# Kernel optimization log

Measured on AMD Instinct MI355X. Metric: run time of the kernel, lower is better.

## Reference

```python
import jax, jax.numpy as jnp
import numpy as np

MARGIN = 0.3
NEG_FILL = -100.0
EPS = 1e-6


def setup_inputs() -> dict:
    key = jax.random.key(0)
    k1, k2, k3 = jax.random.split(key, 3)
    B, N, D = 256, 131072, 128
    xembs = jax.random.normal(k1, (B, D), dtype=jnp.float32)
    yembs = jax.random.normal(k2, (N, D), dtype=jnp.float32)
    pos_inds = jax.random.randint(k3, (B, 1), 0, N, dtype=jnp.int64)
    # target: multi-hot label matrix; positives marked 1 at pos_inds
    target = jnp.zeros((B, N), dtype=jnp.float32)
    target = target.at[jnp.arange(B)[:, None], pos_inds].set(1.0)
    return {"xembs": xembs, "yembs": yembs, "target": target,
            "pos_inds": pos_inds, "num_neg": 5}


def reference(xembs, yembs, target, pos_inds, num_neg):
    # sim: [B, N]
    sim = xembs @ yembs.T
    # positive similarities: [B, 1]
    sim_p = jnp.take_along_axis(sim, pos_inds, axis=1)
    # mask out positives, mine hardest negatives
    neg_sim = jnp.where(target < EPS, sim, NEG_FILL)
    _, idx = jax.lax.top_k(neg_sim, num_neg)          # [B, num_neg]
    sim_n = jnp.take_along_axis(sim, idx, axis=1)      # [B, num_neg]
    # hinge triplet loss
    loss = jnp.maximum(jnp.zeros_like(sim_n), sim_n - sim_p + MARGIN)
    mask = (loss != 0).astype(loss.dtype)
    prob = jax.nn.softmax(sim_n * mask, axis=1)
    return (loss * prob).mean()
```

## Files before the change

kernel.cpp:

```cpp
#include <hip/hip_runtime.h>

#define BROWS 256
#define NCOLS 131072
#define DDIM  128
#define K     5
#define MARGIN 0.3f

#define NBLK   512
#define CPB    (NCOLS / NBLK)
#define NIT    (CPB / 16)
#define TSTR   260

typedef __attribute__((ext_vector_type(8))) __bf16 bf16x8;
typedef __attribute__((ext_vector_type(8))) unsigned short us8;
typedef __attribute__((ext_vector_type(4))) float f32x4;

__device__ __forceinline__ unsigned short f2b(float f) {
    union { float f; unsigned u; } x; x.f = f;
    unsigned r = x.u + 0x7FFFu + ((x.u >> 16) & 1u);
    return (unsigned short)(r >> 16);
}

__device__ __forceinline__ bf16x8 cvt8(const float4& lo, const float4& hi) {
    us8 t;
    t[0] = f2b(lo.x); t[1] = f2b(lo.y); t[2] = f2b(lo.z); t[3] = f2b(lo.w);
    t[4] = f2b(hi.x); t[5] = f2b(hi.y); t[6] = f2b(hi.z); t[7] = f2b(hi.w);
    return __builtin_bit_cast(bf16x8, t);
}

__global__ __launch_bounds__(256, 2) void gemm_topk_kernel(
    const float* __restrict__ x, const float* __restrict__ y,
    const int* __restrict__ pos,
    float* __restrict__ cand_v, float* __restrict__ simp)
{
    __shared__ float simT[16 * TSTR];

    const int tid   = threadIdx.x;
    const int lane  = tid & 63;
    const int quad  = lane >> 4;
    const int l15   = lane & 15;
    const int wrow0 = tid & 192;
    const int col0  = blockIdx.x * CPB;

    bf16x8 af[4][4];
#pragma unroll
    for (int mt = 0; mt < 4; ++mt) {
        const float* xp = x + (size_t)(wrow0 + mt * 16 + l15) * DDIM + quad * 8;
#pragma unroll
        for (int s = 0; s < 4; ++s) {
            const float4 a0 = *(const float4*)(xp + s * 32);
            const float4 a1 = *(const float4*)(xp + s * 32 + 4);
            af[mt][s] = cvt8(a0, a1);
        }
    }

    const int myPos = pos[tid];
    float t5[K];
#pragma unroll
    for (int p = 0; p < K; ++p) t5[p] = -3.0e38f;

    const float* yb = y + (size_t)(col0 + l15) * DDIM + quad * 8;

    float4 cur[8], nxt[8];
#pragma unroll
    for (int s = 0; s < 4; ++s) {
        cur[2 * s]     = *(const float4*)(yb + s * 32);
        cur[2 * s + 1] = *(const float4*)(yb + s * 32 + 4);
    }

    for (int it = 0; it < NIT; ++it) {
        if (it + 1 < NIT) {
            const float* yn = yb + (size_t)(it + 1) * 16 * DDIM;
#pragma unroll
            for (int s = 0; s < 4; ++s) {
                nxt[2 * s]     = *(const float4*)(yn + s * 32);
                nxt[2 * s + 1] = *(const float4*)(yn + s * 32 + 4);
            }
        }

        bf16x8 bfrag[4];
#pragma unroll
        for (int s = 0; s < 4; ++s) bfrag[s] = cvt8(cur[2 * s], cur[2 * s + 1]);

        f32x4 acc[4];
#pragma unroll
        for (int mt = 0; mt < 4; ++mt) acc[mt] = (f32x4){0.f, 0.f, 0.f, 0.f};
#pragma unroll
        for (int s = 0; s < 4; ++s)
#pragma unroll
            for (int mt = 0; mt < 4; ++mt)
                acc[mt] = __builtin_amdgcn_mfma_f32_16x16x32_bf16(af[mt][s], bfrag[s], acc[mt], 0, 0, 0);

        {
            float* wp = &simT[l15 * TSTR + wrow0 + quad * 4];
#pragma unroll
            for (int mt = 0; mt < 4; ++mt)
                *(f32x4*)(wp + mt * 16) = acc[mt];
        }

        const int colbase = col0 + it * 16;
#pragma unroll
        for (int c = 0; c < 16; ++c) {
            const float v = simT[c * TSTR + tid];
            const int col = colbase + c;
            if (col == myPos) {
                simp[tid] = v;
            } else if (v > t5[K - 1]) {
                float nv = v;
#pragma unroll
                for (int p = 0; p < K; ++p) {
                    const bool gt = nv > t5[p];
                    const float tv = t5[p];
                    if (gt) { t5[p] = nv; nv = tv; }
                }
            }
        }

#pragma unroll
        for (int i = 0; i < 8; ++i) cur[i] = nxt[i];
    }

    float* cv = cand_v + ((size_t)blockIdx.x * BROWS + tid) * K;
#pragma unroll
    for (int p = 0; p < K; ++p) cv[p] = t5[p];
}

__device__ __forceinline__ void merge5(float* __restrict__ t5, const float* __restrict__ src) {
#pragma unroll
    for (int p = 0; p < K; ++p) {
        const float v = src[p];
        if (v > t5[K - 1]) {
            float nv = v;
#pragma unroll
            for (int u = 0; u < K; ++u) {
                const bool gt = nv > t5[u];
                const float tv = t5[u];
                if (gt) { t5[u] = nv; nv = tv; }
            }
        }
    }
}

__global__ __launch_bounds__(256) void reduce_kernel(
    const float* __restrict__ cand_v, const float* __restrict__ simp,
    float* __restrict__ row_loss)
{
    const int row = blockIdx.x;
    const int tid = threadIdx.x;
    __shared__ float sv[256 * K];

    float t5[K];
#pragma unroll
    for (int p = 0; p < K; ++p) t5[p] = -3.0e38f;

    merge5(t5, cand_v + ((size_t)tid * BROWS + row) * K);
    merge5(t5, cand_v + ((size_t)(tid + 256) * BROWS + row) * K);

#pragma unroll
    for (int p = 0; p < K; ++p) sv[tid * K + p] = t5[p];
    __syncthreads();

    for (int s = 128; s >= 1; s >>= 1) {
        if (tid < s) {
            merge5(t5, &sv[(tid + s) * K]);
#pragma unroll
            for (int p = 0; p < K; ++p) sv[tid * K + p] = t5[p];
        }
        __syncthreads();
    }

    if (tid == 0) {
        const float sp = simp[row];
        float loss[K], logit[K];
#pragma unroll
        for (int p = 0; p < K; ++p) {
            loss[p]  = fmaxf(0.f, t5[p] - sp + MARGIN);
            logit[p] = (loss[p] != 0.f) ? t5[p] : 0.f;
        }
        float mx = logit[0];
#pragma unroll
        for (int p = 1; p < K; ++p) mx = fmaxf(mx, logit[p]);
        float den = 0.f, num = 0.f;
#pragma unroll
        for (int p = 0; p < K; ++p) {
            const float e = __expf(logit[p] - mx);
            den += e;
            num += loss[p] * e;
        }
        row_loss[row] = num / den;
    }
}

__global__ __launch_bounds__(256) void final_kernel(const float* __restrict__ row_loss,
                                                    float* __restrict__ out)
{
    const int tid = threadIdx.x;
    __shared__ float red[256];
    red[tid] = row_loss[tid];
    __syncthreads();
    for (int s = 128; s >= 1; s >>= 1) {
        if (tid < s) red[tid] += red[tid + s];
        __syncthreads();
    }
    if (tid == 0) out[0] = red[0] * (1.0f / (BROWS * K));
}

extern "C" void kernel_launch(void* const* d_in, const int* in_sizes, int n_in,
                              void* d_out, int out_size, void* d_ws, size_t ws_size,
                              hipStream_t stream) {
    const float* x  = (const float*)d_in[0];
    const float* y  = (const float*)d_in[1];
    const int* pos  = (const int*)d_in[3];

    float* cand_v   = (float*)d_ws;
    float* simp     = cand_v + (size_t)NBLK * BROWS * K;
    float* row_loss = simp + BROWS;

    gemm_topk_kernel<<<dim3(NBLK), 256, 0, stream>>>(x, y, pos, cand_v, simp);
    reduce_kernel<<<dim3(BROWS), 256, 0, stream>>>(cand_v, simp, row_loss);
    final_kernel<<<dim3(1), 256, 0, stream>>>(row_loss, (float*)d_out);
}
```

Before: 246.0 us.

## Pre-convert embeddings to bf16, deepen prefetch, restructure top-k scan and fuse final reduction

A separate kernel converts y and x to bf16 once, so the GEMM kernel streams half the bytes and does no per-tile conversion. The fp32 prefetch pair becomes a 4-deep register ring, and the tile is stored row-major in shared memory so each thread scans its row with float4 loads and a max pre-check. The candidate layout is transposed to give coalesced reads in the reduce, and the final kernel is replaced by an atomicAdd after a memset. The cost is an extra pass that reads and writes all of y, plus a nondeterministic atomic summation order.

Result: slower. 256.0 us (+4.1%).

```diff
diff --git a/kernel.cpp b/kernel.cpp
--- a/kernel.cpp
+++ b/kernel.cpp
@@ -9,7 +9,8 @@
 #define NBLK   512
 #define CPB    (NCOLS / NBLK)
 #define NIT    (CPB / 16)
-#define TSTR   260
+#define RSTR   20
+#define DEPTH  4
 
 typedef __attribute__((ext_vector_type(8))) __bf16 bf16x8;
 typedef __attribute__((ext_vector_type(8))) unsigned short us8;
@@ -21,19 +22,35 @@
     return (unsigned short)(r >> 16);
 }
 
-__device__ __forceinline__ bf16x8 cvt8(const float4& lo, const float4& hi) {
+__global__ __launch_bounds__(256) void convert_kernel(
+    const float* __restrict__ y, const float* __restrict__ x,
+    unsigned short* __restrict__ yb, unsigned short* __restrict__ xb)
+{
+    const int gid = blockIdx.x * 256 + threadIdx.x;
+    const int NY = NCOLS * DDIM / 8;
+    const float* src;
+    unsigned short* dst;
+    int idx;
+    if (gid < NY) { src = y; dst = yb; idx = gid; }
+    else {
+        idx = gid - NY;
+        if (idx >= BROWS * DDIM / 8) return;
+        src = x; dst = xb;
+    }
+    const float4 a = *(const float4*)(src + (size_t)idx * 8);
+    const float4 b = *(const float4*)(src + (size_t)idx * 8 + 4);
     us8 t;
-    t[0] = f2b(lo.x); t[1] = f2b(lo.y); t[2] = f2b(lo.z); t[3] = f2b(lo.w);
-    t[4] = f2b(hi.x); t[5] = f2b(hi.y); t[6] = f2b(hi.z); t[7] = f2b(hi.w);
-    return __builtin_bit_cast(bf16x8, t);
+    t[0] = f2b(a.x); t[1] = f2b(a.y); t[2] = f2b(a.z); t[3] = f2b(a.w);
+    t[4] = f2b(b.x); t[5] = f2b(b.y); t[6] = f2b(b.z); t[7] = f2b(b.w);
+    *(us8*)(dst + (size_t)idx * 8) = t;
 }
 
 __global__ __launch_bounds__(256, 2) void gemm_topk_kernel(
-    const float* __restrict__ x, const float* __restrict__ y,
+    const unsigned short* __restrict__ xb, const unsigned short* __restrict__ yb,
     const int* __restrict__ pos,
     float* __restrict__ cand_v, float* __restrict__ simp)
 {
-    __shared__ float simT[16 * TSTR];
+    __shared__ float simT[BROWS * RSTR];
 
     const int tid   = threadIdx.x;
     const int lane  = tid & 63;
@@ -45,13 +62,10 @@
     bf16x8 af[4][4];
 #pragma unroll
     for (int mt = 0; mt < 4; ++mt) {
-        const float* xp = x + (size_t)(wrow0 + mt * 16 + l15) * DDIM + quad * 8;
-#pragma unroll
-        for (int s = 0; s < 4; ++s) {
-            const float4 a0 = *(const float4*)(xp + s * 32);
-            const float4 a1 = *(const float4*)(xp + s * 32 + 4);
-            af[mt][s] = cvt8(a0, a1);
-        }
+        const unsigned short* xp = xb + (size_t)(wrow0 + mt * 16 + l15) * DDIM + quad * 8;
+#pragma unroll
+        for (int s = 0; s < 4; ++s)
+            af[mt][s] = __builtin_bit_cast(bf16x8, *(const us8*)(xp + s * 32));
     }
 
     const int myPos = pos[tid];
@@ -59,68 +73,74 @@
 #pragma unroll
     for (int p = 0; p < K; ++p) t5[p] = -3.0e38f;
 
-    const float* yb = y + (size_t)(col0 + l15) * DDIM + quad * 8;
-
-    float4 cur[8], nxt[8];
-#pragma unroll
-    for (int s = 0; s < 4; ++s) {
-        cur[2 * s]     = *(const float4*)(yb + s * 32);
-        cur[2 * s + 1] = *(const float4*)(yb + s * 32 + 4);
-    }
-
-    for (int it = 0; it < NIT; ++it) {
-        if (it + 1 < NIT) {
-            const float* yn = yb + (size_t)(it + 1) * 16 * DDIM;
+    const unsigned short* ybase = yb + (size_t)(col0 + l15) * DDIM + quad * 8;
+
+    us8 buf[DEPTH][4];
+#pragma unroll
+    for (int d = 0; d < DEPTH; ++d)
+#pragma unroll
+        for (int s = 0; s < 4; ++s)
+            buf[d][s] = *(const us8*)(ybase + (size_t)d * 16 * DDIM + s * 32);
+
+    for (int it0 = 0; it0 < NIT; it0 += DEPTH) {
+#pragma unroll
+        for (int d = 0; d < DEPTH; ++d) {
+            const int it = it0 + d;
+
+            f32x4 acc[4];
+#pragma unroll
+            for (int mt = 0; mt < 4; ++mt) acc[mt] = (f32x4){0.f, 0.f, 0.f, 0.f};
 #pragma unroll
             for (int s = 0; s < 4; ++s) {
-                nxt[2 * s]     = *(const float4*)(yn + s * 32);
-                nxt[2 * s + 1] = *(const float4*)(yn + s * 32 + 4);
-            }
-        }
-
-        bf16x8 bfrag[4];
-#pragma unroll
-        for (int s = 0; s < 4; ++s) bfrag[s] = cvt8(cur[2 * s], cur[2 * s + 1]);
-
-        f32x4 acc[4];
-#pragma unroll
-        for (int mt = 0; mt < 4; ++mt) acc[mt] = (f32x4){0.f, 0.f, 0.f, 0.f};
-#pragma unroll
-        for (int s = 0; s < 4; ++s)
+                const bf16x8 bf = __builtin_bit_cast(bf16x8, buf[d][s]);
+#pragma unroll
+                for (int mt = 0; mt < 4; ++mt)
+                    acc[mt] = __builtin_amdgcn_mfma_f32_16x16x32_bf16(af[mt][s], bf, acc[mt], 0, 0, 0);
+            }
+
+            {
+                int pf = it + DEPTH; if (pf > NIT - 1) pf = NIT - 1;
+                const unsigned short* yp = ybase + (size_t)pf * 16 * DDIM;
+#pragma unroll
+                for (int s = 0; s < 4; ++s)
+                    buf[d][s] = *(const us8*)(yp + s * 32);
+            }
+
 #pragma unroll
             for (int mt = 0; mt < 4; ++mt)
-                acc[mt] = __builtin_amdgcn_mfma_f32_16x16x32_bf16(af[mt][s], bfrag[s], acc[mt], 0, 0, 0);
-
-        {
-            float* wp = &simT[l15 * TSTR + wrow0 + quad * 4];
-#pragma unroll
-            for (int mt = 0; mt < 4; ++mt)
-                *(f32x4*)(wp + mt * 16) = acc[mt];
-        }
-
-        const int colbase = col0 + it * 16;
-#pragma unroll
-        for (int c = 0; c < 16; ++c) {
-            const float v = simT[c * TSTR + tid];
-            const int col = colbase + c;
-            if (col == myPos) {
-                simp[tid] = v;
-            } else if (v > t5[K - 1]) {
-                float nv = v;
-#pragma unroll
-                for (int p = 0; p < K; ++p) {
-                    const bool gt = nv > t5[p];
-                    const float tv = t5[p];
-                    if (gt) { t5[p] = nv; nv = tv; }
+#pragma unroll
+                for (int r = 0; r < 4; ++r)
+                    simT[(wrow0 + mt * 16 + quad * 4 + r) * RSTR + l15] = acc[mt][r];
+
+            const int colbase = col0 + it * 16;
+            if ((unsigned)(myPos - colbase) < 16u)
+                simp[tid] = simT[tid * RSTR + (myPos - colbase)];
+
+#pragma unroll
+            for (int c4 = 0; c4 < 4; ++c4) {
+                const float4 v = *(const float4*)&simT[tid * RSTR + c4 * 4];
+                const float m = fmaxf(fmaxf(v.x, v.y), fmaxf(v.z, v.w));
+                if (m > t5[K - 1]) {
+                    const float vv[4] = {v.x, v.y, v.z, v.w};
+#pragma unroll
+                    for (int j = 0; j < 4; ++j) {
+                        const int col = colbase + c4 * 4 + j;
+                        if (vv[j] > t5[K - 1] && col != myPos) {
+                            float nv = vv[j];
+#pragma unroll
+                            for (int p = 0; p < K; ++p) {
+                                const bool gt = nv > t5[p];
+                                const float tv = t5[p];
+                                if (gt) { t5[p] = nv; nv = tv; }
+                            }
+                        }
+                    }
                 }
             }
         }
-
-#pragma unroll
-        for (int i = 0; i < 8; ++i) cur[i] = nxt[i];
-    }
-
-    float* cv = cand_v + ((size_t)blockIdx.x * BROWS + tid) * K;
+    }
+
+    float* cv = cand_v + ((size_t)tid * NBLK + blockIdx.x) * K;
 #pragma unroll
     for (int p = 0; p < K; ++p) cv[p] = t5[p];
 }
@@ -143,7 +163,7 @@
 
 __global__ __launch_bounds__(256) void reduce_kernel(
     const float* __restrict__ cand_v, const float* __restrict__ simp,
-    float* __restrict__ row_loss)
+    float* __restrict__ out)
 {
     const int row = blockIdx.x;
     const int tid = threadIdx.x;
@@ -153,8 +173,8 @@
 #pragma unroll
     for (int p = 0; p < K; ++p) t5[p] = -3.0e38f;
 
-    merge5(t5, cand_v + ((size_t)tid * BROWS + row) * K);
-    merge5(t5, cand_v + ((size_t)(tid + 256) * BROWS + row) * K);
+    merge5(t5, cand_v + ((size_t)row * NBLK + tid) * K);
+    merge5(t5, cand_v + ((size_t)row * NBLK + tid + 256) * K);
 
 #pragma unroll
     for (int p = 0; p < K; ++p) sv[tid * K + p] = t5[p];
@@ -187,22 +207,8 @@
             den += e;
             num += loss[p] * e;
         }
-        row_loss[row] = num / den;
-    }
-}
-
-__global__ __launch_bounds__(256) void final_kernel(const float* __restrict__ row_loss,
-                                                    float* __restrict__ out)
-{
-    const int tid = threadIdx.x;
-    __shared__ float red[256];
-    red[tid] = row_loss[tid];
-    __syncthreads();
-    for (int s = 128; s >= 1; s >>= 1) {
-        if (tid < s) red[tid] += red[tid + s];
-        __syncthreads();
-    }
-    if (tid == 0) out[0] = red[0] * (1.0f / (BROWS * K));
+        atomicAdd(out, num / den * (1.0f / (BROWS * K)));
+    }
 }
 
 extern "C" void kernel_launch(void* const* d_in, const int* in_sizes, int n_in,
@@ -212,11 +218,15 @@
     const float* y  = (const float*)d_in[1];
     const int* pos  = (const int*)d_in[3];
 
-    float* cand_v   = (float*)d_ws;
-    float* simp     = cand_v + (size_t)NBLK * BROWS * K;
-    float* row_loss = simp + BROWS;
-
-    gemm_topk_kernel<<<dim3(NBLK), 256, 0, stream>>>(x, y, pos, cand_v, simp);
-    reduce_kernel<<<dim3(BROWS), 256, 0, stream>>>(cand_v, simp, row_loss);
-    final_kernel<<<dim3(1), 256, 0, stream>>>(row_loss, (float*)d_out);
-}
+    unsigned short* yb = (unsigned short*)d_ws;
+    unsigned short* xb = yb + (size_t)NCOLS * DDIM;
+    float* cand_v      = (float*)(xb + (size_t)BROWS * DDIM);
+    float* simp        = cand_v + (size_t)BROWS * NBLK * K;
+
+    hipMemsetAsync(d_out, 0, sizeof(float), stream);
+
+    const int NY = NCOLS * DDIM / 8, NX = BROWS * DDIM / 8;
+    convert_kernel<<<dim3((NY + NX) / 256), 256, 0, stream>>>(y, x, yb, xb);
+    gemm_topk_kernel<<<dim3(NBLK), 256, 0, stream>>>(xb, yb, pos, cand_v, simp);
+    reduce_kernel<<<dim3(BROWS), 256, 0, stream>>>(cand_v, simp, (float*)d_out);
+}
```
